# Optimization experiments

Hardware: AMD Instinct MI355X
Metric: run time of the kernel (lower is better)

## Reference

```python
import jax, jax.numpy as jnp
import numpy as np
from jax import lax

BN_EPS = 1e-5


def ste_sign(t):
    # sign() binarization with straight-through estimator (identity grad),
    # matching BinarizeConv2d which binarizes .data in-place.
    return t + lax.stop_gradient(jnp.sign(t) - t)


def setup_inputs() -> dict:
    key = jax.random.key(0)
    k1, k2, k3, k4 = jax.random.split(key, 4)
    N, C, H, W = 128, 256, 28, 28
    x = jax.random.normal(k1, (N, C, H, W), dtype=jnp.float32)
    w = jax.random.normal(k2, (C, C, 3, 3), dtype=jnp.float32)  # OIHW
    gamma = jnp.ones((C,), dtype=jnp.float32)
    beta = jnp.zeros((C,), dtype=jnp.float32)
    running_mean = jax.random.normal(k3, (C,), dtype=jnp.float32)
    running_var = jax.random.uniform(k4, (C,), dtype=jnp.float32)
    return {"x": x, "w": w, "gamma": gamma, "beta": beta,
            "running_mean": running_mean, "running_var": running_var}


def reference(x, w, gamma, beta, running_mean, running_var):
    residual = x
    # Binarize activations and weights to {-1, 0, +1} via sign (0 measure-zero for randn)
    xb = ste_sign(x)
    wb = ste_sign(w)
    # 3x3 conv, stride 1, padding 1, no bias
    out = lax.conv_general_dilated(
        xb, wb, window_strides=(1, 1), padding=((1, 1), (1, 1)),
        dimension_numbers=("NCHW", "OIHW", "NCHW"))
    # BatchNorm2d (inference form with running stats), per-channel affine
    inv = gamma / jnp.sqrt(running_var + BN_EPS)  # [C]
    out = out * inv[None, :, None, None] + (beta - running_mean * inv)[None, :, None, None]
    # Hardtanh
    out = jnp.clip(out, -1.0, 1.0)
    # residual add (downsample is None)
    return out + residual
```

## Files before the change

kernel.cpp:

```cpp
#include <hip/hip_runtime.h>
#include <stdint.h>

typedef unsigned long long u64;

#define N_ 128
#define C_ 256
#define H_ 28
#define W_ 28
#define BN_EPS_ 1e-5f

__global__ __launch_bounds__(256) void pack_x_kernel(const float* __restrict__ x,
                                                     u64* __restrict__ xbits) {
    int gid  = blockIdx.x * blockDim.x + threadIdx.x;
    int wave = gid >> 6;
    int lane = gid & 63;
    int k    = wave & 3;
    int nh   = wave >> 2;
    if (nh >= N_ * H_) return;
    int h = nh % H_;
    int n = nh / H_;
    int c = k * 64 + lane;
    const float* xp = x + (((size_t)n * C_ + c) * H_ + h) * W_;

    u64 my = 0;
    #pragma unroll
    for (int w = 0; w < W_; ++w) {
        u64 mask = __ballot(xp[w] < 0.f);
        if (lane == w) my = mask;
    }
    if (lane < W_) xbits[((size_t)nh * W_ + lane) * 4 + k] = my;
}

__global__ __launch_bounds__(256) void pack_w_kernel(const float* __restrict__ w,
                                                     u64* __restrict__ wbits) {
    int gid  = blockIdx.x * blockDim.x + threadIdx.x;
    int wave = gid >> 6;
    int lane = gid & 63;
    if (wave >= C_ * 9 * 4) return;
    int k    = wave & 3;
    int rest = wave >> 2;
    int tap  = rest % 9;
    int co   = rest / 9;
    int ci   = k * 64 + lane;
    float val = w[((size_t)co * C_ + ci) * 9 + tap];
    u64 mask = __ballot(val < 0.f);
    if (lane == 0) wbits[wave] = mask;
}

__global__ __launch_bounds__(256) void conv_kernel(
    const u64* __restrict__ xbits, const u64* __restrict__ wbits,
    const float* __restrict__ x,
    const float* __restrict__ gamma, const float* __restrict__ beta,
    const float* __restrict__ mean, const float* __restrict__ var,
    float* __restrict__ out) {
    int nh = blockIdx.x;
    int h  = nh % H_;
    int n  = nh / H_;
    int co = threadIdx.x;

    __shared__ union {
        u64   lx[3][W_][4];
        float sout[C_][29];
    } sm;

    float inv  = gamma[co] / sqrtf(var[co] + BN_EPS_);
    float bias = beta[co] - mean[co] * inv;

    u64 wr[9][4];
    {
        const ulonglong2* wp = (const ulonglong2*)wbits + (size_t)co * 18;
        #pragma unroll
        for (int i = 0; i < 9; ++i) {
            ulonglong2 a = wp[i * 2];
            ulonglong2 b = wp[i * 2 + 1];
            wr[i][0] = a.x; wr[i][1] = a.y; wr[i][2] = b.x; wr[i][3] = b.y;
        }
    }

    for (int i = threadIdx.x; i < 3 * W_ * 4; i += 256) {
        int k    = i & 3;
        int rest = i >> 2;
        int ww   = rest % W_;
        int r    = rest / W_;
        int ih   = h - 1 + r;
        u64 v = 0;
        if (ih >= 0 && ih < H_)
            v = xbits[(((size_t)n * H_ + ih) * W_ + ww) * 4 + k];
        sm.lx[r][ww][k] = v;
    }
    __syncthreads();

    const bool row0 = (h > 0);
    const bool row2 = (h < H_ - 1);
    const int  nrows = 1 + (row0 ? 1 : 0) + (row2 ? 1 : 0);

    int sacc[W_];
    int pm = 0, pc = 0;

    for (int iw = 0; iw < W_; ++iw) {
        int a0 = 0, a1 = 0, a2 = 0;
        u64 xw0, xw1, xw2, xw3;
        #define TAPROW(r, wb)                                                  \
            xw0 = sm.lx[r][iw][0]; xw1 = sm.lx[r][iw][1];                      \
            xw2 = sm.lx[r][iw][2]; xw3 = sm.lx[r][iw][3];                      \
            a0 += __popcll(xw0 ^ wr[wb+0][0]) + __popcll(xw1 ^ wr[wb+0][1]) +  \
                  __popcll(xw2 ^ wr[wb+0][2]) + __popcll(xw3 ^ wr[wb+0][3]);   \
            a1 += __popcll(xw0 ^ wr[wb+1][0]) + __popcll(xw1 ^ wr[wb+1][1]) +  \
                  __popcll(xw2 ^ wr[wb+1][2]) + __popcll(xw3 ^ wr[wb+1][3]);   \
            a2 += __popcll(xw0 ^ wr[wb+2][0]) + __popcll(xw1 ^ wr[wb+2][1]) +  \
                  __popcll(xw2 ^ wr[wb+2][2]) + __popcll(xw3 ^ wr[wb+2][3]);
        if (row0) { TAPROW(0, 0) }
        { TAPROW(1, 3) }
        if (row2) { TAPROW(2, 6) }
        #undef TAPROW
        if (iw >= 1) sacc[iw - 1] = pm + a2;
        pm = pc + a1;
        pc = a0;
    }
    sacc[W_ - 1] = pm;

    __syncthreads();

    #pragma unroll
    for (int w = 0; w < W_; ++w) {
        int ncols = 3 - (w == 0 ? 1 : 0) - (w == W_ - 1 ? 1 : 0);
        int nv    = C_ * nrows * ncols;
        float convv = (float)(nv - 2 * sacc[w]);
        float val   = convv * inv + bias;
        val = fminf(1.f, fmaxf(-1.f, val));
        sm.sout[co][w] = val;
    }
    __syncthreads();

    const float* xplane = x   + ((size_t)n * C_ * H_ + h) * W_;
    float*       oplane = out + ((size_t)n * C_ * H_ + h) * W_;
    for (int i = threadIdx.x; i < C_ * W_; i += 256) {
        int c    = i / W_;
        int wpos = i - c * W_;
        size_t g = (size_t)c * (H_ * W_) + wpos;
        oplane[g] = sm.sout[c][wpos] + xplane[g];
    }
}

extern "C" void kernel_launch(void* const* d_in, const int* in_sizes, int n_in,
                              void* d_out, int out_size, void* d_ws, size_t ws_size,
                              hipStream_t stream) {
    const float* x     = (const float*)d_in[0];
    const float* w     = (const float*)d_in[1];
    const float* gamma = (const float*)d_in[2];
    const float* beta  = (const float*)d_in[3];
    const float* mean  = (const float*)d_in[4];
    const float* var   = (const float*)d_in[5];
    float* out = (float*)d_out;

    u64* xbits = (u64*)d_ws;
    u64* wbits = xbits + (size_t)N_ * H_ * W_ * 4;

    int pack_x_threads = N_ * H_ * 4 * 64;
    pack_x_kernel<<<(pack_x_threads + 255) / 256, 256, 0, stream>>>(x, xbits);
    pack_w_kernel<<<(C_ * 9 * 4 * 64) / 256, 256, 0, stream>>>(w, wbits);
    conv_kernel<<<N_ * H_, 256, 0, stream>>>(xbits, wbits, x, gamma, beta, mean, var, out);
}
```

Before: 327.9 us.

## Stage x rows through shared memory in pack kernel and fuse BN epilogue into conv loop

The x packing kernel now loads each (n,h) row across all channels with coalesced float4 reads into shared memory before balloting sign bits, replacing strided per-lane scalar loads. The conv kernel drops the per-thread sacc register array and applies BN, hardtanh and the shared-memory store inline as each output column completes. It also splits the former shared-memory union into separate buffers and adds a min-blocks launch bound of 2. Together these aim to cut uncoalesced global traffic and register pressure, at the cost of more shared memory per block.

```diff
diff --git a/kernel.cpp b/kernel.cpp
--- a/kernel.cpp
+++ b/kernel.cpp
@@ -11,21 +11,29 @@
 
 __global__ __launch_bounds__(256) void pack_x_kernel(const float* __restrict__ x,
                                                      u64* __restrict__ xbits) {
-    int gid  = blockIdx.x * blockDim.x + threadIdx.x;
-    int wave = gid >> 6;
-    int lane = gid & 63;
-    int k    = wave & 3;
-    int nh   = wave >> 2;
-    if (nh >= N_ * H_) return;
-    int h = nh % H_;
-    int n = nh / H_;
-    int c = k * 64 + lane;
-    const float* xp = x + (((size_t)n * C_ + c) * H_ + h) * W_;
+    int nh = blockIdx.x;
+    int h  = nh % H_;
+    int n  = nh / H_;
+    __shared__ float sx[C_][W_ + 1];
 
+    const float* xplane = x + ((size_t)n * C_ * H_ + h) * W_;
+    for (int i = threadIdx.x; i < C_ * 7; i += 256) {
+        int c = i / 7, q = i - c * 7;
+        float4 v = *(const float4*)(xplane + (size_t)c * (H_ * W_) + q * 4);
+        sx[c][q * 4 + 0] = v.x;
+        sx[c][q * 4 + 1] = v.y;
+        sx[c][q * 4 + 2] = v.z;
+        sx[c][q * 4 + 3] = v.w;
+    }
+    __syncthreads();
+
+    int k    = threadIdx.x >> 6;
+    int lane = threadIdx.x & 63;
+    int c    = k * 64 + lane;
     u64 my = 0;
     #pragma unroll
     for (int w = 0; w < W_; ++w) {
-        u64 mask = __ballot(xp[w] < 0.f);
+        u64 mask = __ballot(sx[c][w] < 0.f);
         if (lane == w) my = mask;
     }
     if (lane < W_) xbits[((size_t)nh * W_ + lane) * 4 + k] = my;
@@ -47,7 +55,7 @@
     if (lane == 0) wbits[wave] = mask;
 }
 
-__global__ __launch_bounds__(256) void conv_kernel(
+__global__ __launch_bounds__(256, 2) void conv_kernel(
     const u64* __restrict__ xbits, const u64* __restrict__ wbits,
     const float* __restrict__ x,
     const float* __restrict__ gamma, const float* __restrict__ beta,
@@ -58,10 +66,8 @@
     int n  = nh / H_;
     int co = threadIdx.x;
 
-    __shared__ union {
-        u64   lx[3][W_][4];
-        float sout[C_][29];
-    } sm;
+    __shared__ u64   lx[3][W_][4];
+    __shared__ float sout[C_][W_ + 1];
 
     float inv  = gamma[co] / sqrtf(var[co] + BN_EPS_);
     float bias = beta[co] - mean[co] * inv;
@@ -86,23 +92,24 @@
         u64 v = 0;
         if (ih >= 0 && ih < H_)
             v = xbits[(((size_t)n * H_ + ih) * W_ + ww) * 4 + k];
-        sm.lx[r][ww][k] = v;
+        lx[r][ww][k] = v;
     }
     __syncthreads();
 
     const bool row0 = (h > 0);
     const bool row2 = (h < H_ - 1);
     const int  nrows = 1 + (row0 ? 1 : 0) + (row2 ? 1 : 0);
+    const int  nv3 = C_ * nrows * 3;
+    const int  nv2 = C_ * nrows * 2;
 
-    int sacc[W_];
     int pm = 0, pc = 0;
 
     for (int iw = 0; iw < W_; ++iw) {
         int a0 = 0, a1 = 0, a2 = 0;
         u64 xw0, xw1, xw2, xw3;
         #define TAPROW(r, wb)                                                  \
-            xw0 = sm.lx[r][iw][0]; xw1 = sm.lx[r][iw][1];                      \
-            xw2 = sm.lx[r][iw][2]; xw3 = sm.lx[r][iw][3];                      \
+            xw0 = lx[r][iw][0]; xw1 = lx[r][iw][1];                            \
+            xw2 = lx[r][iw][2]; xw3 = lx[r][iw][3];                            \
             a0 += __popcll(xw0 ^ wr[wb+0][0]) + __popcll(xw1 ^ wr[wb+0][1]) +  \
                   __popcll(xw2 ^ wr[wb+0][2]) + __popcll(xw3 ^ wr[wb+0][3]);   \
             a1 += __popcll(xw0 ^ wr[wb+1][0]) + __popcll(xw1 ^ wr[wb+1][1]) +  \
@@ -113,22 +120,21 @@
         { TAPROW(1, 3) }
         if (row2) { TAPROW(2, 6) }
         #undef TAPROW
-        if (iw >= 1) sacc[iw - 1] = pm + a2;
+
+        if (iw >= 1) {
+            int s  = pm + a2;
+            int nv = (iw == 1) ? nv2 : nv3;
+            float val = (float)(nv - 2 * s) * inv + bias;
+            val = fminf(1.f, fmaxf(-1.f, val));
+            sout[co][iw - 1] = val;
+        }
         pm = pc + a1;
         pc = a0;
     }
-    sacc[W_ - 1] = pm;
-
-    __syncthreads();
-
-    #pragma unroll
-    for (int w = 0; w < W_; ++w) {
-        int ncols = 3 - (w == 0 ? 1 : 0) - (w == W_ - 1 ? 1 : 0);
-        int nv    = C_ * nrows * ncols;
-        float convv = (float)(nv - 2 * sacc[w]);
-        float val   = convv * inv + bias;
+    {
+        float val = (float)(nv2 - 2 * pm) * inv + bias;
         val = fminf(1.f, fmaxf(-1.f, val));
-        sm.sout[co][w] = val;
+        sout[co][W_ - 1] = val;
     }
     __syncthreads();
 
@@ -138,7 +144,7 @@
         int c    = i / W_;
         int wpos = i - c * W_;
         size_t g = (size_t)c * (H_ * W_) + wpos;
-        oplane[g] = sm.sout[c][wpos] + xplane[g];
+        oplane[g] = sout[c][wpos] + xplane[g];
     }
 }
 
@@ -156,8 +162,7 @@
     u64* xbits = (u64*)d_ws;
     u64* wbits = xbits + (size_t)N_ * H_ * W_ * 4;
 
-    int pack_x_threads = N_ * H_ * 4 * 64;
-    pack_x_kernel<<<(pack_x_threads + 255) / 256, 256, 0, stream>>>(x, xbits);
+    pack_x_kernel<<<N_ * H_, 256, 0, stream>>>(x, xbits);
     pack_w_kernel<<<(C_ * 9 * 4 * 64) / 256, 256, 0, stream>>>(w, wbits);
     conv_kernel<<<N_ * H_, 256, 0, stream>>>(xbits, wbits, x, gamma, beta, mean, var, out);
 }
```

Result: no change. 328.8 us (+0.3%).
